# Kernel tuning notes

Hardware: AMD Instinct MI355X
Metric: run time of the kernel (lower is better)

Reference implementation:

```python
import jax, jax.numpy as jnp
import numpy as np

N = 100000      # nodes
E = 1600000     # edges (before self-loops)
FIN = 128       # in_channels
HID = 16        # hidden_channels
H = 8           # heads (layer 1)
OUT = 64        # out_channels
LN_EPS = 1e-5


def setup_inputs() -> dict:
    key = jax.random.key(0)
    ks = jax.random.split(key, 24)
    def p(i, shape):
        return jax.random.normal(ks[i], shape, dtype=jnp.float32) * 0.05
    return {
        "x": jax.random.normal(ks[0], (N, FIN), dtype=jnp.float32),
        "edge_index": jax.random.randint(ks[1], (2, E), 0, N, dtype=jnp.int32),
        # GATv2 layer 1: in -> H*HID, concat
        "Wl1": p(2, (FIN, H * HID)), "bl1": p(3, (H * HID,)),
        "Wr1": p(4, (FIN, H * HID)), "br1": p(5, (H * HID,)),
        "att1": p(6, (H, HID)), "bias1": p(7, (H * HID,)),
        # GATv2 layer 2: H*HID -> HID, heads=1
        "Wl2": p(8, (H * HID, HID)), "bl2": p(9, (HID,)),
        "Wr2": p(10, (H * HID, HID)), "br2": p(11, (HID,)),
        "att2": p(12, (1, HID)), "bias2": p(13, (HID,)),
        # LayerNorms
        "ln1_g": jnp.ones((H * HID,), jnp.float32), "ln1_b": jnp.zeros((H * HID,), jnp.float32),
        "ln2_g": jnp.ones((HID,), jnp.float32), "ln2_b": jnp.zeros((HID,), jnp.float32),
        # residual / skip / output linears
        "res1_W": p(14, (FIN, H * HID)), "res1_b": p(15, (H * HID,)),
        "res2_W": p(16, (H * HID, HID)), "res2_b": p(17, (HID,)),
        "skip_W": p(18, (H * HID, HID)), "skip_b": p(19, (HID,)),
        "out_W": p(20, (HID, OUT)), "out_b": p(21, (OUT,)),
    }


def _layernorm(x, g, b):
    mu = jnp.mean(x, axis=-1, keepdims=True)
    var = jnp.mean((x - mu) ** 2, axis=-1, keepdims=True)
    return (x - mu) * jax.lax.rsqrt(var + LN_EPS) * g + b


def _gatv2(x, src, dst, Wl, bl, Wr, br, att, bias, concat):
    # PyG GATv2Conv (share_weights=False, eval mode): message from src j to dst i
    Hh, C = att.shape
    n = x.shape[0]
    xl = (x @ Wl + bl).reshape(n, Hh, C)   # source-side transform
    xr = (x @ Wr + br).reshape(n, Hh, C)   # target-side transform
    m = xl[src] + xr[dst]                  # [E, H, C]
    e = jax.nn.leaky_relu(m, 0.2)
    alpha = jnp.einsum('ehc,hc->eh', e, att)          # [E, H]
    amax = jax.ops.segment_max(alpha, dst, num_segments=n)
    alpha = jnp.exp(alpha - amax[dst])
    denom = jax.ops.segment_sum(alpha, dst, num_segments=n)
    alpha = alpha / (denom[dst] + 1e-16)
    out = jax.ops.segment_sum(xl[src] * alpha[:, :, None], dst, num_segments=n)  # [N, H, C]
    out = out.reshape(n, Hh * C) if concat else out.mean(axis=1)
    return out + bias


def reference(x, edge_index, Wl1, bl1, Wr1, br1, att1, bias1,
              Wl2, bl2, Wr2, br2, att2, bias2,
              ln1_g, ln1_b, ln2_g, ln2_b,
              res1_W, res1_b, res2_W, res2_b, skip_W, skip_b, out_W, out_b):
    n = x.shape[0]
    loops = jnp.arange(n, dtype=edge_index.dtype)
    src = jnp.concatenate([edge_index[0], loops])
    dst = jnp.concatenate([edge_index[1], loops])

    h = _gatv2(x, src, dst, Wl1, bl1, Wr1, br1, att1, bias1, concat=True)
    h = _layernorm(h, ln1_g, ln1_b)
    h = h + (x @ res1_W + res1_b)
    h = jax.nn.elu(h)            # dropout off in eval

    skip_in = h
    h2 = _gatv2(h, src, dst, Wl2, bl2, Wr2, br2, att2, bias2, concat=False)
    h2 = _layernorm(h2, ln2_g, ln2_b)
    h2 = h2 + (skip_in @ res2_W + res2_b)
    h2 = jax.nn.elu(h2)
    h2 = h2 + (skip_in @ skip_W + skip_b)
    return h2 @ out_W + out_b
```

## Files before the change

### kernel.cpp

```cpp
#include <hip/hip_runtime.h>

typedef __attribute__((ext_vector_type(8))) short bf16x8;
typedef __attribute__((ext_vector_type(4))) float f32x4;

__device__ __forceinline__ float bf2f(ushort u) {
  union { uint i; float f; } v; v.i = ((uint)u) << 16; return v.f;
}
__device__ __forceinline__ ushort f2bf(float f) {
  union { float f; uint i; } v; v.f = f;
  uint r = (v.i + 0x7FFFu + ((v.i >> 16) & 1u)) >> 16;
  return (ushort)r;
}
__device__ __forceinline__ float blo(uint u) { return __builtin_bit_cast(float, u << 16); }
__device__ __forceinline__ float bhi(uint u) { return __builtin_bit_cast(float, u & 0xffff0000u); }

template <int CTRL>
__device__ __forceinline__ float dppadd(float x) {
  union { float f; int i; } a, b;
  a.f = x;
  b.i = __builtin_amdgcn_update_dpp(0, a.i, CTRL, 0xF, 0xF, true);
  return a.f + b.f;
}
#define DPP_X1 0xB1
#define DPP_X2 0x4E
#define DPP_X7 0x141
#define DPP_XF 0x140


__global__ __launch_bounds__(256) void k_init(
    const float* __restrict__ Wl1, const float* __restrict__ bl1,
    const float* __restrict__ Wr1, const float* __restrict__ br1,
    const float* __restrict__ res1W, const float* __restrict__ res1b,
    const float* __restrict__ Wl2, const float* __restrict__ bl2,
    const float* __restrict__ Wr2, const float* __restrict__ br2,
    const float* __restrict__ res2W, const float* __restrict__ res2b,
    const float* __restrict__ skipW, const float* __restrict__ skipb,
    const float* __restrict__ att1, const float* __restrict__ att2,
    ushort* __restrict__ W1F, float* __restrict__ B1P,
    ushort* __restrict__ W2F, float* __restrict__ B2P,
    float* __restrict__ at6, float* __restrict__ at4, float* __restrict__ at2E,
    int* __restrict__ cnt, int N) {
  const float LOG2E = 1.4426950408889634f;
  int b = blockIdx.x, t = threadIdx.x;
  if (b < 227) {
    int tid = b * 256 + t;
    if (tid < 49152) {
      int j = tid & 7, l = (tid >> 3) & 63, ktile = (tid >> 9) & 3, ct = tid >> 11;
      int k = ktile * 32 + ((l >> 4) << 3) + j;
      int n = ct * 16 + (l & 15);
      int sel = n >> 7, jj = n & 127;
      const float* s = sel == 0 ? Wl1 : sel == 1 ? Wr1 : res1W;
      W1F[tid] = f2bf(s[k * 128 + jj]);
    } else if (tid < 57344) {
      int u = tid - 49152;
      int j = u & 7, l = (u >> 3) & 63, ktile = (u >> 9) & 3, ct = u >> 11;
      int k = ktile * 32 + ((l >> 4) << 3) + j;
      int n = ct * 16 + (l & 15);
      int sel = n >> 4, jj = n & 15;
      const float* s = sel == 0 ? Wl2 : sel == 1 ? Wr2 : sel == 2 ? res2W : skipW;
      W2F[u] = f2bf(s[k * 16 + jj]);
    } else if (tid < 57728) {
      int n = tid - 57344;
      int sel = n >> 7, jj = n & 127;
      const float* sb = sel == 0 ? bl1 : sel == 1 ? br1 : res1b;
      B1P[n] = sb[jj];
    } else if (tid < 57792) {
      int n = tid - 57728;
      int sel = n >> 4, jj = n & 15;
      const float* sb = sel == 0 ? bl2 : sel == 1 ? br2 : sel == 2 ? res2b : skipb;
      B2P[n] = sb[jj];
    } else if (tid < 57920) {
      int n = tid - 57792;
      at6[n] = att1[n] * 0.6f * LOG2E;
    } else if (tid < 58048) {
      int n = tid - 57920;
      at4[n] = att1[n] * 0.4f * LOG2E;
    } else if (tid < 58064) {
      int n = tid - 58048;
      at2E[n] = att2[n] * LOG2E;
    }
  } else {
    int idx = (b - 227) * 256 + t;
    if (idx < N) cnt[idx] = 0;
  }
}


__global__ __launch_bounds__(256) void k_histgemm(
    const int* __restrict__ ei, int* __restrict__ cnt, int E, int nh,
    const float* __restrict__ x, const ushort* __restrict__ WF,
    const float* __restrict__ bias,
    ushort* __restrict__ O0, ushort* __restrict__ O1, ushort* __restrict__ O2,
    int M) {
  __shared__ ushort LT[64 * 392];
  int b = blockIdx.x, t = threadIdx.x;
  if (b < nh) {
    int e4 = (b * 256 + t) * 4;
    if (e4 + 3 < E) {
      int4 d = *(const int4*)&ei[E + e4];
      atomicAdd(&cnt[d.x], 1); atomicAdd(&cnt[d.y], 1);
      atomicAdd(&cnt[d.z], 1); atomicAdd(&cnt[d.w], 1);
    } else {
      for (int e = e4; e < E; ++e) atomicAdd(&cnt[ei[E + e]], 1);
    }
    return;
  }
  int w = t >> 6, l = t & 63;
  int m0 = (b - nh) * 64;
  int rql = l & 15, kq = l >> 4;
  bf16x8 afr[16];
  #pragma unroll
  for (int kt = 0; kt < 4; ++kt) {
    #pragma unroll
    for (int rt = 0; rt < 4; ++rt) {
      int m = m0 + rt * 16 + rql;
      uint4 o = make_uint4(0, 0, 0, 0);
      if (m < M) {
        const float* src = x + (size_t)m * 128 + kt * 32 + kq * 8;
        float4 f0 = *(const float4*)src;
        float4 f1 = *(const float4*)(src + 4);
        o.x = f2bf(f0.x) | ((uint)f2bf(f0.y) << 16);
        o.y = f2bf(f0.z) | ((uint)f2bf(f0.w) << 16);
        o.z = f2bf(f1.x) | ((uint)f2bf(f1.y) << 16);
        o.w = f2bf(f1.z) | ((uint)f2bf(f1.w) << 16);
      }
      afr[kt * 4 + rt] = __builtin_bit_cast(bf16x8, o);
    }
  }
  #pragma unroll
  for (int ct6 = 0; ct6 < 6; ++ct6) {
    int ct = w * 6 + ct6;
    int col = ct * 16 + rql;
    float bv = bias[col];
    f32x4 acc[4] = {};
    #pragma unroll
    for (int kt = 0; kt < 4; ++kt) {
      bf16x8 bfrag = *(const bf16x8*)(WF + ((size_t)((ct * 4 + kt) * 64 + l)) * 8);
      #pragma unroll
      for (int rt = 0; rt < 4; ++rt)
        acc[rt] = __builtin_amdgcn_mfma_f32_16x16x32_bf16(afr[kt * 4 + rt], bfrag, acc[rt], 0, 0, 0);
    }
    #pragma unroll
    for (int rt = 0; rt < 4; ++rt)
      #pragma unroll
      for (int r = 0; r < 4; ++r)
        LT[(rt * 16 + kq * 4 + r) * 392 + col] = f2bf(acc[rt][r] + bv);
  }
  __syncthreads();
  #pragma unroll
  for (int a = 0; a < 3; ++a) {
    ushort* O = a == 0 ? O0 : a == 1 ? O1 : O2;
    #pragma unroll
    for (int it = 0; it < 4; ++it) {
      int idx = it * 256 + t;
      int row = idx >> 4, seg = idx & 15;
      int m = m0 + row;
      if (m < M) {
        uint4 v = *(const uint4*)&LT[row * 392 + a * 128 + seg * 8];
        *(uint4*)&O[(size_t)m * 128 + seg * 8] = v;
      }
    }
  }
}


__global__ __launch_bounds__(256) void k_scan1(const int* __restrict__ cnt, int* __restrict__ partial, int n) {
  int i = blockIdx.x * 256 + threadIdx.x;
  int v = (i < n) ? cnt[i] : 0;
  #pragma unroll
  for (int m = 1; m < 64; m <<= 1) v += __shfl_xor(v, m);
  __shared__ int sm[4];
  if ((threadIdx.x & 63) == 0) sm[threadIdx.x >> 6] = v;
  __syncthreads();
  if (threadIdx.x == 0) partial[blockIdx.x] = sm[0] + sm[1] + sm[2] + sm[3];
}


__global__ __launch_bounds__(256) void k_scan3lb(const int* __restrict__ cnt, const int* __restrict__ partial,
                                                 int* __restrict__ rowptr, int* __restrict__ cursor, int n) {
  int t = threadIdx.x;
  int b = blockIdx.x;
  int acc = 0;
  for (int j = t; j < b; j += 256) acc += partial[j];
  #pragma unroll
  for (int m = 1; m < 64; m <<= 1) acc += __shfl_xor(acc, m);
  __shared__ int sm[4];
  if ((t & 63) == 0) sm[t >> 6] = acc;
  __syncthreads();
  int base = sm[0] + sm[1] + sm[2] + sm[3];
  __shared__ int buf[2][256];
  int i = b * 256 + t;
  int v = (i < n) ? cnt[i] : 0;
  buf[0][t] = v;
  __syncthreads();
  int cur = 0;
  for (int off = 1; off < 256; off <<= 1) {
    int x = buf[cur][t];
    if (t >= off) x += buf[cur][t - off];
    buf[cur ^ 1][t] = x;
    __syncthreads();
    cur ^= 1;
  }
  if (i < n) {
    int incl = buf[cur][t];
    int rp = base + incl - v;
    rowptr[i] = rp;
    cursor[i] = rp;
    if (i == n - 1) rowptr[n] = base + incl;
  }
}


__global__ __launch_bounds__(256) void k_scatter(const int* __restrict__ ei, int* __restrict__ cursor,
                                                 int* __restrict__ ssrc, int E, int NS) {
  int t = threadIdx.x;
  int base = blockIdx.x * 2048;
  int src[8], dst[8];
  #pragma unroll
  for (int j = 0; j < 8; ++j) {
    int idx = base + j * 256 + t;
    bool ok = idx < E;
    src[j] = ok ? ei[idx] : 0;
    dst[j] = ok ? ei[E + idx] : -1;
  }
  for (int s = 0; s < NS; ++s) {
    #pragma unroll
    for (int j = 0; j < 8; ++j) {
      if ((dst[j] >> 13) == s) {
        int pos = atomicAdd(&cursor[dst[j]], 1);
        ssrc[pos] = src[j];
      }
    }
  }
}


__global__ __launch_bounds__(256) void k_mfma2(
    const ushort* __restrict__ AF, const ushort* __restrict__ WF,
    const float* __restrict__ bias,
    ushort* __restrict__ O0, ushort* __restrict__ O1,
    ushort* __restrict__ O2, ushort* __restrict__ O3, int M) {
  int w = threadIdx.x >> 6, l = threadIdx.x & 63;
  int m0 = blockIdx.x * 64;
  int c0 = w * 16;
  int ct = c0 >> 4;
  f32x4 acc[4] = {};
  #pragma unroll
  for (int kt = 0; kt < 4; ++kt) {
    bf16x8 b = *(const bf16x8*)(WF + ((size_t)((ct * 4 + kt) * 64 + l)) * 8);
    #pragma unroll
    for (int rt = 0; rt < 4; ++rt) {
      bf16x8 a = *(const bf16x8*)(AF + ((size_t)((blockIdx.x * 16 + rt * 4 + kt) * 64 + l)) * 8);
      acc[rt] = __builtin_amdgcn_mfma_f32_16x16x32_bf16(a, b, acc[rt], 0, 0, 0);
    }
  }
  int col = c0 + (l & 15);
  int arr = col >> 4;
  ushort* O = arr == 0 ? O0 : arr == 1 ? O1 : arr == 2 ? O2 : O3;
  int lcol = col & 15;
  float bv = bias[col];
  int rbase = m0 + ((l >> 4) << 2);
  #pragma unroll
  for (int rt = 0; rt < 4; ++rt) {
    #pragma unroll
    for (int r = 0; r < 4; ++r) {
      int m = rbase + rt * 16 + r;
      if (m < M) O[(size_t)m * 16 + lcol] = f2bf(acc[rt][r] + bv);
    }
  }
}


#define EDGE1B(u, MASKHI)                                              \
  {                                                                    \
    float v0 = blo((u).x), v1 = bhi((u).x);                            \
    float v2 = blo((u).y), v3 = bhi((u).y);                            \
    float m0 = v0 + xr0, m1 = v1 + xr1, m2 = v2 + xr2, m3 = v3 + xr3;  \
    float d = a6.x * m0 + a4.x * __builtin_fabsf(m0);                  \
    d += a6.y * m1; d += a4.y * __builtin_fabsf(m1);                   \
    d += a6.z * m2; d += a4.z * __builtin_fabsf(m2);                   \
    d += a6.w * m3; d += a4.w * __builtin_fabsf(m3);                   \
    d = dppadd<DPP_X1>(d);                                             \
    d = dppadd<DPP_X2>(d);                                             \
    float p = __builtin_amdgcn_exp2f(d);                               \
    if (MASKHI) p = hi ? 0.f : p;                                      \
    acc0 += p * v0; acc1 += p * v1; acc2 += p * v2; acc3 += p * v3;    \
    den += p;                                                          \
  }

__global__ __launch_bounds__(256) void k_gat1(
    const ushort* __restrict__ XLG, const ushort* __restrict__ XR,
    const ushort* __restrict__ RE,
    const float* __restrict__ at6, const float* __restrict__ at4,
    const float* __restrict__ bias1,
    const float* __restrict__ g1, const float* __restrict__ b1,
    const int* __restrict__ rowptr, const int* __restrict__ ssrc,
    ushort* __restrict__ HF, int n) {
  int lane = threadIdx.x & 63;
  int i = blockIdx.x * 4 + (threadIdx.x >> 6);
  if (i >= n) return;
  int l32 = lane & 31;
  bool hi = lane >= 32;
  int hioff4 = (lane & 32) >> 3;
  int fbb = l32 << 3;
  int fb = l32 * 4;
  size_t rowb = (size_t)i << 8;
  uint2 uxr = *(const uint2*)((const char*)XR + rowb + fbb);
  float xr0 = blo(uxr.x), xr1 = bhi(uxr.x), xr2 = blo(uxr.y), xr3 = bhi(uxr.y);
  float4 a6 = *(const float4*)&at6[fb];
  float4 a4 = *(const float4*)&at4[fb];
  float acc0 = 0.f, acc1 = 0.f, acc2 = 0.f, acc3 = 0.f, den = 0.f;
  {
    uint2 us = *(const uint2*)((const char*)XLG + rowb + fbb);
    EDGE1B(us, true);
  }
  int e0 = __builtin_amdgcn_readfirstlane(rowptr[i]);
  int e1 = __builtin_amdgcn_readfirstlane(rowptr[i + 1]);
  for (int base = e0; base < e1; base += 64) {
    int cnt = e1 - base; if (cnt > 64) cnt = 64;
    int sidx = ssrc[base + (lane < cnt ? lane : cnt - 1)];
    int j = 0;
    for (; j + 8 <= cnt; j += 8) {
      uint o0 = (uint)__builtin_amdgcn_ds_bpermute(((j + 0) << 2) + hioff4, sidx) << 8;
      uint o1 = (uint)__builtin_amdgcn_ds_bpermute(((j + 2) << 2) + hioff4, sidx) << 8;
      uint o2 = (uint)__builtin_amdgcn_ds_bpermute(((j + 4) << 2) + hioff4, sidx) << 8;
      uint o3 = (uint)__builtin_amdgcn_ds_bpermute(((j + 6) << 2) + hioff4, sidx) << 8;
      uint2 u0 = *(const uint2*)((const char*)XLG + o0 + fbb);
      uint2 u1 = *(const uint2*)((const char*)XLG + o1 + fbb);
      uint2 u2 = *(const uint2*)((const char*)XLG + o2 + fbb);
      uint2 u3 = *(const uint2*)((const char*)XLG + o3 + fbb);
      EDGE1B(u0, false); EDGE1B(u1, false); EDGE1B(u2, false); EDGE1B(u3, false);
    }
    for (; j + 2 <= cnt; j += 2) {
      uint o = (uint)__builtin_amdgcn_ds_bpermute((j << 2) + hioff4, sidx) << 8;
      uint2 u = *(const uint2*)((const char*)XLG + o + fbb);
      EDGE1B(u, false);
    }
    if (j < cnt) {
      uint o = (uint)__builtin_amdgcn_ds_bpermute((j << 2) + hioff4, sidx) << 8;
      uint2 u = *(const uint2*)((const char*)XLG + o + fbb);
      EDGE1B(u, true);
    }
  }
  acc0 += __shfl_xor(acc0, 32);
  acc1 += __shfl_xor(acc1, 32);
  acc2 += __shfl_xor(acc2, 32);
  acc3 += __shfl_xor(acc3, 32);
  den  += __shfl_xor(den, 32);
  float inv = 1.f / (den + 1e-16f);
  float4 bv = *(const float4*)&bias1[fb];
  float o0 = acc0 * inv + bv.x, o1 = acc1 * inv + bv.y;
  float o2 = acc2 * inv + bv.z, o3 = acc3 * inv + bv.w;
  float s = o0 + o1 + o2 + o3;
  #pragma unroll
  for (int m = 1; m < 32; m <<= 1) s += __shfl_xor(s, m);
  float mu = s * (1.f / 128.f);
  float d0 = o0 - mu, d1 = o1 - mu, d2 = o2 - mu, d3 = o3 - mu;
  float q = d0 * d0 + d1 * d1 + d2 * d2 + d3 * d3;
  #pragma unroll
  for (int m = 1; m < 32; m <<= 1) q += __shfl_xor(q, m);
  float rstd = rsqrtf(q * (1.f / 128.f) + 1e-5f);
  float4 gg = *(const float4*)&g1[fb];
  float4 bb = *(const float4*)&b1[fb];
  uint2 ur = *(const uint2*)((const char*)RE + rowb + fbb);
  float r0 = blo(ur.x), r1 = bhi(ur.x), r2 = blo(ur.y), r3 = bhi(ur.y);
  float y0 = d0 * rstd * gg.x + bb.x + r0;
  float y1 = d1 * rstd * gg.y + bb.y + r1;
  float y2 = d2 * rstd * gg.z + bb.z + r2;
  float y3 = d3 * rstd * gg.w + bb.w + r3;
  y0 = y0 > 0.f ? y0 : __expf(y0) - 1.f;
  y1 = y1 > 0.f ? y1 : __expf(y1) - 1.f;
  y2 = y2 > 0.f ? y2 : __expf(y2) - 1.f;
  y3 = y3 > 0.f ? y3 : __expf(y3) - 1.f;
  if (!hi) {
    int k8 = l32 >> 1;
    size_t slot = ((size_t)(i >> 4) * 4 + (k8 >> 2)) * 64 + (i & 15) + ((k8 & 3) << 4);
    uint2 o;
    o.x = (uint)f2bf(y0) | ((uint)f2bf(y1) << 16);
    o.y = (uint)f2bf(y2) | ((uint)f2bf(y3) << 16);
    *(uint2*)(HF + slot * 8 + (l32 & 1) * 4) = o;
  }
}


#define EDGE2V(v)                                            \
  {                                                          \
    float m = (v) + xr;                                      \
    float ta = a2 * m;                                       \
    float tb = a2 * __builtin_fabsf(m);                      \
    float tt = 0.6f * ta + 0.4f * tb;                        \
    tt = dppadd<DPP_X1>(tt);                                 \
    tt = dppadd<DPP_X2>(tt);                                 \
    tt = dppadd<DPP_X7>(tt);                                 \
    tt = dppadd<DPP_XF>(tt);                                 \
    float p = __builtin_amdgcn_exp2f(tt);                    \
    acc += p * (v); den += p;                                \
  }

__global__ __launch_bounds__(256) void k_gat2(
    const ushort* __restrict__ XG, const ushort* __restrict__ XRr,
    const ushort* __restrict__ XE, const ushort* __restrict__ XS,
    const float* __restrict__ at2E, const float* __restrict__ bias2,
    const float* __restrict__ g2, const float* __restrict__ b2,
    const int* __restrict__ rowptr, const int* __restrict__ ssrc,
    const float* __restrict__ outW, const float* __restrict__ outB,
    float* __restrict__ Out, int n) {
  __shared__ float sW[1024];
  __shared__ float sB[64];
  int t = threadIdx.x;
  for (int idx = t; idx < 1024; idx += 256) sW[idx] = outW[idx];
  if (t < 64) sB[t] = outB[t];
  __syncthreads();
  int c = t & 15;
  int i = blockIdx.x * 16 + (t >> 4);
  if (i >= n) return;
  size_t ib = (size_t)i << 4;
  float xl = bf2f(XG[ib + c]), xr = bf2f(XRr[ib + c]);
  float resv = bf2f(XE[ib + c]), skipv = bf2f(XS[ib + c]);
  float a2 = at2E[c];
  float acc = 0.f, den = 0.f;
  EDGE2V(xl);
  int e0 = rowptr[i], e1 = rowptr[i + 1];
  int e = e0;
  for (; e + 8 <= e1; e += 8) {
    int s0 = ssrc[e],     s1 = ssrc[e + 1], s2 = ssrc[e + 2], s3 = ssrc[e + 3];
    int s4 = ssrc[e + 4], s5 = ssrc[e + 5], s6 = ssrc[e + 6], s7 = ssrc[e + 7];
    float v0 = bf2f(XG[((size_t)(uint)s0 << 4) + c]);
    float v1 = bf2f(XG[((size_t)(uint)s1 << 4) + c]);
    float v2 = bf2f(XG[((size_t)(uint)s2 << 4) + c]);
    float v3 = bf2f(XG[((size_t)(uint)s3 << 4) + c]);
    float v4 = bf2f(XG[((size_t)(uint)s4 << 4) + c]);
    float v5 = bf2f(XG[((size_t)(uint)s5 << 4) + c]);
    float v6 = bf2f(XG[((size_t)(uint)s6 << 4) + c]);
    float v7 = bf2f(XG[((size_t)(uint)s7 << 4) + c]);
    EDGE2V(v0); EDGE2V(v1); EDGE2V(v2); EDGE2V(v3);
    EDGE2V(v4); EDGE2V(v5); EDGE2V(v6); EDGE2V(v7);
  }
  for (; e < e1; ++e) {
    int s = ssrc[e];
    float v = bf2f(XG[((size_t)(uint)s << 4) + c]);
    EDGE2V(v);
  }
  float o = acc / (den + 1e-16f) + bias2[c];
  float s = o;
  s = dppadd<DPP_X1>(s); s = dppadd<DPP_X2>(s); s = dppadd<DPP_X7>(s); s = dppadd<DPP_XF>(s);
  float mu = s * (1.f / 16.f);
  float d = o - mu;
  float q = d * d;
  q = dppadd<DPP_X1>(q); q = dppadd<DPP_X2>(q); q = dppadd<DPP_X7>(q); q = dppadd<DPP_XF>(q);
  float rstd = rsqrtf(q * (1.f / 16.f) + 1e-5f);
  float y = d * rstd * g2[c] + b2[c] + resv;
  y = y > 0.f ? y : __expf(y) - 1.f;
  y += skipv;
  float a0 = sB[c * 4 + 0], a1 = sB[c * 4 + 1], ao2 = sB[c * 4 + 2], a3 = sB[c * 4 + 3];
  #pragma unroll
  for (int cc = 0; cc < 16; ++cc) {
    float h = __shfl(y, cc, 16);
    a0 += h * sW[cc * 64 + c * 4 + 0];
    a1 += h * sW[cc * 64 + c * 4 + 1];
    ao2 += h * sW[cc * 64 + c * 4 + 2];
    a3 += h * sW[cc * 64 + c * 4 + 3];
  }
  *(float4*)&Out[(size_t)i * 64 + c * 4] = make_float4(a0, a1, ao2, a3);
}


extern "C" void kernel_launch(void* const* d_in, const int* in_sizes, int n_in,
                              void* d_out, int out_size, void* d_ws, size_t ws_size,
                              hipStream_t stream) {
  const float* x     = (const float*)d_in[0];
  const int*   ei    = (const int*)d_in[1];
  const float* Wl1   = (const float*)d_in[2];
  const float* bl1   = (const float*)d_in[3];
  const float* Wr1   = (const float*)d_in[4];
  const float* br1   = (const float*)d_in[5];
  const float* att1  = (const float*)d_in[6];
  const float* bias1 = (const float*)d_in[7];
  const float* Wl2   = (const float*)d_in[8];
  const float* bl2   = (const float*)d_in[9];
  const float* Wr2   = (const float*)d_in[10];
  const float* br2   = (const float*)d_in[11];
  const float* att2  = (const float*)d_in[12];
  const float* bias2 = (const float*)d_in[13];
  const float* ln1g  = (const float*)d_in[14];
  const float* ln1b  = (const float*)d_in[15];
  const float* ln2g  = (const float*)d_in[16];
  const float* ln2b  = (const float*)d_in[17];
  const float* res1W = (const float*)d_in[18];
  const float* res1b = (const float*)d_in[19];
  const float* res2W = (const float*)d_in[20];
  const float* res2b = (const float*)d_in[21];
  const float* skipW = (const float*)d_in[22];
  const float* skipb = (const float*)d_in[23];
  const float* outW  = (const float*)d_in[24];
  const float* outb  = (const float*)d_in[25];
  int N = in_sizes[0] / 128;
  int E = in_sizes[1] / 2;
  float* out = (float*)d_out;

  int nblk = (N + 63) / 64;
  int ngrp = nblk * 4;

  ushort* XLG  = (ushort*)d_ws;
  ushort* XR1  = XLG + (size_t)N * 128;
  ushort* RE1  = XR1 + (size_t)N * 128;
  ushort* HF   = RE1 + (size_t)N * 128;
  ushort* XG2  = HF + (size_t)ngrp * 2048;
  ushort* X2R  = XG2 + (size_t)N * 16;
  ushort* X2E  = X2R + (size_t)N * 16;
  ushort* X2S  = X2E + (size_t)N * 16;
  ushort* W1F  = X2S + (size_t)N * 16;
  ushort* W2F  = W1F + 49152;
  float*  B1P  = (float*)(W2F + 8192);
  float*  B2P  = B1P + 384;
  float*  at6  = B2P + 64;
  float*  at4  = at6 + 128;
  float*  at2E = at4 + 128;
  int* cnt     = (int*)(at2E + 16);
  int* cursor  = cnt + N;
  int* rowptr  = cursor + N;
  int* ssrc    = rowptr + N + 1;
  int* partial = ssrc + E;

  int nbS = (N + 255) / 256;
  int NS  = ((N - 1) >> 13) + 1;
  int nScat = (E + 2047) / 2048;
  int nh = (E + 1023) / 1024;

  k_init<<<227 + nbS, 256, 0, stream>>>(Wl1, bl1, Wr1, br1, res1W, res1b,
                                        Wl2, bl2, Wr2, br2, res2W, res2b, skipW, skipb,
                                        att1, att2, W1F, B1P, W2F, B2P, at6, at4, at2E,
                                        cnt, N);
  k_histgemm<<<nh + nblk, 256, 0, stream>>>(ei, cnt, E, nh, x, W1F, B1P,
                                            XLG, XR1, RE1, N);
  k_scan1<<<nbS, 256, 0, stream>>>(cnt, partial, N);
  k_scan3lb<<<nbS, 256, 0, stream>>>(cnt, partial, rowptr, cursor, N);
  k_scatter<<<nScat, 256, 0, stream>>>(ei, cursor, ssrc, E, NS);
  k_gat1<<<(N + 3) / 4, 256, 0, stream>>>(XLG, XR1, RE1, at6, at4, bias1, ln1g, ln1b,
                                          rowptr, ssrc, HF, N);
  k_mfma2<<<nblk, 256, 0, stream>>>(HF, W2F, B2P, XG2, X2R, X2E, X2S, N);
  k_gat2<<<(N + 15) / 16, 256, 0, stream>>>(XG2, X2R, X2E, X2S, at2E, bias2, ln2g, ln2b,
                                            rowptr, ssrc, outW, outb, out, N);
}
```

Measured before the change: 466.2 us.

## Split fused histogram+GEMM kernel and shrink GEMM LDS tile to one output

The fused kernel that ran the degree histogram and the layer-1 input GEMM in one grid is split into two kernels. The GEMM now runs after the scatter, right before gat1, which may keep its outputs warmer in cache for gat1. Its LDS staging buffer shrinks from three outputs at once to one output per pass, with extra barriers, to raise occupancy. The cost is an extra launch and losing the overlap between atomic-heavy histogram blocks and MFMA blocks.

```diff
diff --git a/kernel.cpp b/kernel.cpp
--- a/kernel.cpp
+++ b/kernel.cpp
@@ -86,80 +86,14 @@
 }
 
 
-__global__ __launch_bounds__(256) void k_histgemm(
-    const int* __restrict__ ei, int* __restrict__ cnt, int E, int nh,
-    const float* __restrict__ x, const ushort* __restrict__ WF,
-    const float* __restrict__ bias,
-    ushort* __restrict__ O0, ushort* __restrict__ O1, ushort* __restrict__ O2,
-    int M) {
-  __shared__ ushort LT[64 * 392];
-  int b = blockIdx.x, t = threadIdx.x;
-  if (b < nh) {
-    int e4 = (b * 256 + t) * 4;
-    if (e4 + 3 < E) {
-      int4 d = *(const int4*)&ei[E + e4];
-      atomicAdd(&cnt[d.x], 1); atomicAdd(&cnt[d.y], 1);
-      atomicAdd(&cnt[d.z], 1); atomicAdd(&cnt[d.w], 1);
-    } else {
-      for (int e = e4; e < E; ++e) atomicAdd(&cnt[ei[E + e]], 1);
-    }
-    return;
-  }
-  int w = t >> 6, l = t & 63;
-  int m0 = (b - nh) * 64;
-  int rql = l & 15, kq = l >> 4;
-  bf16x8 afr[16];
-  #pragma unroll
-  for (int kt = 0; kt < 4; ++kt) {
-    #pragma unroll
-    for (int rt = 0; rt < 4; ++rt) {
-      int m = m0 + rt * 16 + rql;
-      uint4 o = make_uint4(0, 0, 0, 0);
-      if (m < M) {
-        const float* src = x + (size_t)m * 128 + kt * 32 + kq * 8;
-        float4 f0 = *(const float4*)src;
-        float4 f1 = *(const float4*)(src + 4);
-        o.x = f2bf(f0.x) | ((uint)f2bf(f0.y) << 16);
-        o.y = f2bf(f0.z) | ((uint)f2bf(f0.w) << 16);
-        o.z = f2bf(f1.x) | ((uint)f2bf(f1.y) << 16);
-        o.w = f2bf(f1.z) | ((uint)f2bf(f1.w) << 16);
-      }
-      afr[kt * 4 + rt] = __builtin_bit_cast(bf16x8, o);
-    }
-  }
-  #pragma unroll
-  for (int ct6 = 0; ct6 < 6; ++ct6) {
-    int ct = w * 6 + ct6;
-    int col = ct * 16 + rql;
-    float bv = bias[col];
-    f32x4 acc[4] = {};
-    #pragma unroll
-    for (int kt = 0; kt < 4; ++kt) {
-      bf16x8 bfrag = *(const bf16x8*)(WF + ((size_t)((ct * 4 + kt) * 64 + l)) * 8);
-      #pragma unroll
-      for (int rt = 0; rt < 4; ++rt)
-        acc[rt] = __builtin_amdgcn_mfma_f32_16x16x32_bf16(afr[kt * 4 + rt], bfrag, acc[rt], 0, 0, 0);
-    }
-    #pragma unroll
-    for (int rt = 0; rt < 4; ++rt)
-      #pragma unroll
-      for (int r = 0; r < 4; ++r)
-        LT[(rt * 16 + kq * 4 + r) * 392 + col] = f2bf(acc[rt][r] + bv);
-  }
-  __syncthreads();
-  #pragma unroll
-  for (int a = 0; a < 3; ++a) {
-    ushort* O = a == 0 ? O0 : a == 1 ? O1 : O2;
-    #pragma unroll
-    for (int it = 0; it < 4; ++it) {
-      int idx = it * 256 + t;
-      int row = idx >> 4, seg = idx & 15;
-      int m = m0 + row;
-      if (m < M) {
-        uint4 v = *(const uint4*)&LT[row * 392 + a * 128 + seg * 8];
-        *(uint4*)&O[(size_t)m * 128 + seg * 8] = v;
-      }
-    }
+__global__ __launch_bounds__(256) void k_hist(const int* __restrict__ ei, int* __restrict__ cnt, int E) {
+  int e4 = (blockIdx.x * 256 + threadIdx.x) * 4;
+  if (e4 + 3 < E) {
+    int4 d = *(const int4*)&ei[E + e4];
+    atomicAdd(&cnt[d.x], 1); atomicAdd(&cnt[d.y], 1);
+    atomicAdd(&cnt[d.z], 1); atomicAdd(&cnt[d.w], 1);
+  } else {
+    for (int e = e4; e < E; ++e) atomicAdd(&cnt[ei[E + e]], 1);
   }
 }
 
@@ -231,6 +165,73 @@
         ssrc[pos] = src[j];
       }
     }
+  }
+}
+
+
+__global__ __launch_bounds__(256) void k_gemm1(
+    const float* __restrict__ x, const ushort* __restrict__ WF,
+    const float* __restrict__ bias,
+    ushort* __restrict__ O0, ushort* __restrict__ O1, ushort* __restrict__ O2,
+    int M) {
+  __shared__ ushort LT[64 * 136];
+  int t = threadIdx.x, w = t >> 6, l = t & 63;
+  int m0 = blockIdx.x * 64;
+  int rql = l & 15, kq = l >> 4;
+  bf16x8 afr[16];
+  #pragma unroll
+  for (int kt = 0; kt < 4; ++kt) {
+    #pragma unroll
+    for (int rt = 0; rt < 4; ++rt) {
+      int m = m0 + rt * 16 + rql;
+      uint4 o = make_uint4(0, 0, 0, 0);
+      if (m < M) {
+        const float* src = x + (size_t)m * 128 + kt * 32 + kq * 8;
+        float4 f0 = *(const float4*)src;
+        float4 f1 = *(const float4*)(src + 4);
+        o.x = f2bf(f0.x) | ((uint)f2bf(f0.y) << 16);
+        o.y = f2bf(f0.z) | ((uint)f2bf(f0.w) << 16);
+        o.z = f2bf(f1.x) | ((uint)f2bf(f1.y) << 16);
+        o.w = f2bf(f1.z) | ((uint)f2bf(f1.w) << 16);
+      }
+      afr[kt * 4 + rt] = __builtin_bit_cast(bf16x8, o);
+    }
+  }
+  #pragma unroll
+  for (int a = 0; a < 3; ++a) {
+    #pragma unroll
+    for (int c2 = 0; c2 < 2; ++c2) {
+      int ctl = w * 2 + c2;
+      int ct = a * 8 + ctl;
+      int col = ctl * 16 + rql;
+      float bv = bias[a * 128 + col];
+      f32x4 acc[4] = {};
+      #pragma unroll
+      for (int kt = 0; kt < 4; ++kt) {
+        bf16x8 bfrag = *(const bf16x8*)(WF + ((size_t)((ct * 4 + kt) * 64 + l)) * 8);
+        #pragma unroll
+        for (int rt = 0; rt < 4; ++rt)
+          acc[rt] = __builtin_amdgcn_mfma_f32_16x16x32_bf16(afr[kt * 4 + rt], bfrag, acc[rt], 0, 0, 0);
+      }
+      #pragma unroll
+      for (int rt = 0; rt < 4; ++rt)
+        #pragma unroll
+        for (int r = 0; r < 4; ++r)
+          LT[(rt * 16 + kq * 4 + r) * 136 + col] = f2bf(acc[rt][r] + bv);
+    }
+    __syncthreads();
+    ushort* O = a == 0 ? O0 : a == 1 ? O1 : O2;
+    #pragma unroll
+    for (int it = 0; it < 4; ++it) {
+      int idx = it * 256 + t;
+      int row = idx >> 4, seg = idx & 15;
+      int m = m0 + row;
+      if (m < M) {
+        uint4 v = *(const uint4*)&LT[row * 136 + seg * 8];
+        *(uint4*)&O[(size_t)m * 128 + seg * 8] = v;
+      }
+    }
+    __syncthreads();
   }
 }
 
@@ -525,17 +526,16 @@
   int nbS = (N + 255) / 256;
   int NS  = ((N - 1) >> 13) + 1;
   int nScat = (E + 2047) / 2048;
-  int nh = (E + 1023) / 1024;
 
   k_init<<<227 + nbS, 256, 0, stream>>>(Wl1, bl1, Wr1, br1, res1W, res1b,
                                         Wl2, bl2, Wr2, br2, res2W, res2b, skipW, skipb,
                                         att1, att2, W1F, B1P, W2F, B2P, at6, at4, at2E,
                                         cnt, N);
-  k_histgemm<<<nh + nblk, 256, 0, stream>>>(ei, cnt, E, nh, x, W1F, B1P,
-                                            XLG, XR1, RE1, N);
+  k_hist<<<(E + 1023) / 1024, 256, 0, stream>>>(ei, cnt, E);
   k_scan1<<<nbS, 256, 0, stream>>>(cnt, partial, N);
   k_scan3lb<<<nbS, 256, 0, stream>>>(cnt, partial, rowptr, cursor, N);
   k_scatter<<<nScat, 256, 0, stream>>>(ei, cursor, ssrc, E, NS);
+  k_gemm1<<<nblk, 256, 0, stream>>>(x, W1F, B1P, XLG, XR1, RE1, N);
   k_gat1<<<(N + 3) / 4, 256, 0, stream>>>(XLG, XR1, RE1, at6, at4, bias1, ln1g, ln1b,
                                           rowptr, ssrc, HF, N);
   k_mfma2<<<nblk, 256, 0, stream>>>(HF, W2F, B2P, XG2, X2R, X2E, X2S, N);
```

Result: slower. 478.7 us (+2.7%).
